# Optimization experiments

Measured on AMD Instinct MI355X. Metric: run time of the kernel, lower is better.

## Reference

```python
import jax, jax.numpy as jnp
import numpy as np

B, S, H, D = 2, 2048, 16, 128
HID = H * D
THETA = 10000.0
SCALE = 1.0 / np.sqrt(D)


def setup_inputs() -> dict:
    key = jax.random.key(0)
    k1, k2, k3 = jax.random.split(key, 3)
    x = jax.random.normal(k1, (B, S, HID), dtype=jnp.float32)
    w_qkv = jax.random.normal(k2, (3 * HID, HID), dtype=jnp.float32) * 0.02
    w_o = jax.random.normal(k3, (HID, HID), dtype=jnp.float32) * 0.02
    return {"x": x, "w_qkv": w_qkv, "w_o": w_o}


def _rope_cos_sin(seq_len, dim, dtype):
    inv_freq = 1.0 / (THETA ** (jnp.arange(0, dim, 2, dtype=jnp.float32) / dim))
    pos = jnp.arange(seq_len, dtype=jnp.float32)
    freqs = pos[:, None] * inv_freq[None, :]          # (S, D/2)
    emb = jnp.concatenate([freqs, freqs], axis=-1)    # (S, D)
    return jnp.cos(emb).astype(dtype), jnp.sin(emb).astype(dtype)


def _rotate_half(t):
    t1, t2 = jnp.split(t, 2, axis=-1)
    return jnp.concatenate([-t2, t1], axis=-1)


def reference(x, w_qkv, w_o):
    b, s, _ = x.shape
    qkv = jnp.einsum('bsh,oh->bso', x, w_qkv)                 # (B,S,3*HID)
    qkv = qkv.reshape(b, s, 3, H, D).transpose(2, 0, 3, 1, 4)  # (3,B,H,S,D)
    q, k, v = qkv[0], qkv[1], qkv[2]
    cos, sin = _rope_cos_sin(s, D, x.dtype)                    # (S,D)
    q = q * cos + _rotate_half(q) * sin
    k = k * cos + _rotate_half(k) * sin
    scores = jnp.einsum('bhqd,bhkd->bhqk', q, k) * SCALE       # (B,H,S,S)
    causal = jnp.triu(jnp.ones((s, s), dtype=bool), k=1)
    scores = jnp.where(causal[None, None], -jnp.inf, scores)
    attn = jax.nn.softmax(scores.astype(jnp.float32), axis=-1).astype(q.dtype)
    out = jnp.einsum('bhqk,bhkd->bhqd', attn, v)               # (B,H,S,D)
    out = out.transpose(0, 2, 1, 3).reshape(b, s, HID)
    return jnp.einsum('bsh,oh->bso', out, w_o)
```

## Files before the change

kernel.cpp:

```cpp
#include <hip/hip_runtime.h>
#include <hip/hip_bf16.h>

typedef unsigned short u16;
typedef unsigned long long u64;
typedef u16 us8 __attribute__((ext_vector_type(8)));
typedef __bf16 bf8_t __attribute__((ext_vector_type(8)));
typedef float f32x4 __attribute__((ext_vector_type(4)));

__device__ __forceinline__ float b2f(u16 u) {
    return __uint_as_float(((unsigned int)u) << 16);
}
__device__ __forceinline__ u16 f2b(float f) {
    union { __hip_bfloat16 h; u16 u; } v;
    v.h = __float2bfloat16(f);
    return v.u;
}
__device__ __forceinline__ f32x4 mfma16(bf8_t a, bf8_t b, f32x4 c) {
    return __builtin_amdgcn_mfma_f32_16x16x32_bf16(a, b, c, 0, 0, 0);
}
__device__ __forceinline__ void gload_lds16(const u16* g, u16* lds_base) {
    __builtin_amdgcn_global_load_lds((const __attribute__((address_space(1))) unsigned int*)g,
                                     (__attribute__((address_space(3))) unsigned int*)lds_base,
                                     16, 0, 0);
}

__global__ __launch_bounds__(256) void f32_to_bf16(const float* __restrict__ src,
                                                   u16* __restrict__ dst, int n8) {
    int idx = blockIdx.x * 256 + threadIdx.x;
    if (idx >= n8) return;
    float4 f0 = ((const float4*)src)[idx * 2];
    float4 f1 = ((const float4*)src)[idx * 2 + 1];
    us8 o;
    o[0] = f2b(f0.x); o[1] = f2b(f0.y); o[2] = f2b(f0.z); o[3] = f2b(f0.w);
    o[4] = f2b(f1.x); o[5] = f2b(f1.y); o[6] = f2b(f1.z); o[7] = f2b(f1.w);
    ((us8*)dst)[idx] = o;
}

template<int STORE_F32>
__global__ __launch_bounds__(256) void gemm_mfma_bt(const u16* __restrict__ A, const u16* __restrict__ B,
                                                    void* __restrict__ Cout, int M, int N, int K, int ldc) {
    __shared__ u16 Alds[128 * 32];
    __shared__ u16 Blds[128 * 32];
    const int tid = threadIdx.x;
    const int lane = tid & 63, wave = tid >> 6;
    const int lm = lane & 15, lq = lane >> 4;
    const int wm = wave >> 1, wn = wave & 1;
    const int m0 = blockIdx.y * 128, n0 = blockIdx.x * 128;
    const int srow = lane >> 2;
    const int scol = (lane & 3) * 8;

    f32x4 acc[4][4] = {};

    for (int k0 = 0; k0 < K; k0 += 32) {
#pragma unroll
        for (int p = 0; p < 2; p++) {
            int rbase = wave * 16 + p * 64;
            gload_lds16(A + (size_t)(m0 + rbase + srow) * K + k0 + scol, &Alds[rbase * 32]);
            gload_lds16(B + (size_t)(n0 + rbase + srow) * K + k0 + scol, &Blds[rbase * 32]);
        }
        __syncthreads();
        bf8_t af[4], bf[4];
#pragma unroll
        for (int mb = 0; mb < 4; mb++)
            af[mb] = *(const bf8_t*)&Alds[(wm * 64 + mb * 16 + lm) * 32 + lq * 8];
#pragma unroll
        for (int nb = 0; nb < 4; nb++)
            bf[nb] = *(const bf8_t*)&Blds[(wn * 64 + nb * 16 + lm) * 32 + lq * 8];
#pragma unroll
        for (int mb = 0; mb < 4; mb++)
#pragma unroll
            for (int nb = 0; nb < 4; nb++)
                acc[mb][nb] = mfma16(af[mb], bf[nb], acc[mb][nb]);
        __syncthreads();
    }
#pragma unroll
    for (int mb = 0; mb < 4; mb++)
#pragma unroll
        for (int nb = 0; nb < 4; nb++)
#pragma unroll
            for (int r = 0; r < 4; r++) {
                int row = m0 + wm * 64 + mb * 16 + lq * 4 + r;
                int col = n0 + wn * 64 + nb * 16 + lm;
                if (STORE_F32)
                    ((float*)Cout)[(size_t)row * ldc + col] = acc[mb][nb][r];
                else
                    ((u16*)Cout)[(size_t)row * ldc + col] = f2b(acc[mb][nb][r]);
            }
}

__global__ __launch_bounds__(256) void rope_bf16(u16* __restrict__ qkv) {
    int idx = blockIdx.x * 256 + threadIdx.x;
    int j = idx & 63;
    int h = (idx >> 6) & 15;
    int s = (idx >> 10) & 2047;
    int b = idx >> 21;
    size_t base = ((size_t)(b * 2048 + s)) * 6144 + h * 128;
    float inv = __expf((float)j * (-9.210340371976184f / 64.f));
    float ang = (float)s * inv;
    float sn, c;
    sincosf(ang, &sn, &c);
    float q1 = b2f(qkv[base + j]), q2 = b2f(qkv[base + j + 64]);
    qkv[base + j]      = f2b(q1 * c - q2 * sn);
    qkv[base + j + 64] = f2b(q2 * c + q1 * sn);
    float k1 = b2f(qkv[base + 2048 + j]), k2 = b2f(qkv[base + 2048 + j + 64]);
    qkv[base + 2048 + j]      = f2b(k1 * c - k2 * sn);
    qkv[base + 2048 + j + 64] = f2b(k2 * c + k1 * sn);
}

__global__ __launch_bounds__(256) void transpose_v(const u16* __restrict__ qkv, u16* __restrict__ VT) {
    __shared__ u16 T[64 * 136];
    const int tid = threadIdx.x;
    const int s0 = blockIdx.x * 64;
    const int bh = blockIdx.y;
    const int b = bh >> 4, h = bh & 15;
#pragma unroll
    for (int p = 0; p < 4; p++) {
        int sl = p * 16 + (tid >> 4);
        int d0 = (tid & 15) * 8;
        *(us8*)&T[sl * 136 + d0] =
            *(const us8*)(qkv + ((size_t)(b * 2048 + s0 + sl)) * 6144 + 4096 + h * 128 + d0);
    }
    __syncthreads();
#pragma unroll
    for (int p = 0; p < 4; p++) {
        int idx = p * 256 + tid;
        int d = idx & 127;
        int sg = idx >> 7;
        us8 v;
#pragma unroll
        for (int i = 0; i < 8; i++) v[i] = T[(sg * 8 + i) * 136 + d];
        *(us8*)&VT[((size_t)bh * 128 + d) * 2048 + s0 + sg * 8] = v;
    }
}

#define ATT_SCALE 0.08838834764831845f

__global__ __launch_bounds__(256) void attn_flash(const u16* __restrict__ qkv, const u16* __restrict__ VT,
                                                  u16* __restrict__ AO) {
    const int bh = blockIdx.x;
    const int qt = 31 - blockIdx.y;
    const int b = bh >> 4, h = bh & 15;
    const int tid = threadIdx.x, lane = tid & 63, wave = tid >> 6;
    const int lm = lane & 15, lq = lane >> 4;
    const int q0 = qt * 64;

    __shared__ u16 Kt[64 * 136];
    __shared__ u16 Vt[128 * 72];

    bf8_t qf[4];
    {
        const u16* Qrow = qkv + ((size_t)(b * 2048 + q0 + wave * 16 + lm)) * 6144 + h * 128;
#pragma unroll
        for (int ks = 0; ks < 4; ks++)
            qf[ks] = *(const bf8_t*)(Qrow + ks * 32 + lq * 8);
    }

    f32x4 Of[8] = {};
    float mrun = -3.0e38f, lrun = 0.f;

    const u16* Kbase = qkv + (size_t)b * 2048 * 6144 + 2048 + h * 128;
    const u16* VTbase = VT + (size_t)bh * 128 * 2048;

    const int krow = tid >> 4;
    const int kcol = (tid & 15) * 8;
    const int vrow = tid >> 3;
    const int vcol = (tid & 7) * 8;

    us8 kreg[4], vreg[4];
#pragma unroll
    for (int p = 0; p < 4; p++) {
        kreg[p] = *(const us8*)(Kbase + (size_t)(p * 16 + krow) * 6144 + kcol);
        vreg[p] = *(const us8*)(VTbase + (size_t)(p * 32 + vrow) * 2048 + vcol);
    }

    for (int kt = 0; kt <= qt; kt++) {
        __syncthreads();
#pragma unroll
        for (int p = 0; p < 4; p++) {
            *(us8*)&Kt[(p * 16 + krow) * 136 + kcol] = kreg[p];
            *(us8*)&Vt[(p * 32 + vrow) * 72 + vcol] = vreg[p];
        }
        __syncthreads();
        {
            int kn = (kt + 1 <= qt ? kt + 1 : qt) * 64;
#pragma unroll
            for (int p = 0; p < 4; p++) {
                kreg[p] = *(const us8*)(Kbase + (size_t)(kn + p * 16 + krow) * 6144 + kcol);
                vreg[p] = *(const us8*)(VTbase + (size_t)(p * 32 + vrow) * 2048 + kn + vcol);
            }
        }

        float sv[4][4];
#pragma unroll
        for (int nb = 0; nb < 4; nb++) {
            f32x4 a = {};
#pragma unroll
            for (int ks = 0; ks < 4; ks++) {
                bf8_t kf = *(const bf8_t*)&Kt[(nb * 16 + lm) * 136 + ks * 32 + lq * 8];
                a = mfma16(kf, qf[ks], a);
            }
#pragma unroll
            for (int r = 0; r < 4; r++) sv[nb][r] = a[r] * ATT_SCALE;
        }
        if (kt == qt) {
            int qloc = wave * 16 + lm;
#pragma unroll
            for (int nb = 0; nb < 4; nb++)
#pragma unroll
                for (int r = 0; r < 4; r++)
                    if (nb * 16 + lq * 4 + r > qloc) sv[nb][r] = -3.0e38f;
        }
        float mx = -3.0e38f;
#pragma unroll
        for (int nb = 0; nb < 4; nb++)
#pragma unroll
            for (int r = 0; r < 4; r++) mx = fmaxf(mx, sv[nb][r]);
        mx = fmaxf(mx, __shfl_xor(mx, 16, 64));
        mx = fmaxf(mx, __shfl_xor(mx, 32, 64));
        float mnew = fmaxf(mrun, mx);
        float alpha = __expf(mrun - mnew);
        float rs = 0.f;
        u64 pk[4];
#pragma unroll
        for (int nb = 0; nb < 4; nb++) {
            float e0 = __expf(sv[nb][0] - mnew), e1 = __expf(sv[nb][1] - mnew);
            float e2 = __expf(sv[nb][2] - mnew), e3 = __expf(sv[nb][3] - mnew);
            rs += (e0 + e1) + (e2 + e3);
            unsigned int lo = (unsigned int)f2b(e0) | ((unsigned int)f2b(e1) << 16);
            unsigned int hi = (unsigned int)f2b(e2) | ((unsigned int)f2b(e3) << 16);
            pk[nb] = (u64)lo | ((u64)hi << 32);
        }
        rs += __shfl_xor(rs, 16, 64);
        rs += __shfl_xor(rs, 32, 64);
        lrun = lrun * alpha + rs;
        mrun = mnew;
#pragma unroll
        for (int db = 0; db < 8; db++)
#pragma unroll
            for (int r = 0; r < 4; r++) Of[db][r] *= alpha;

        const int slo = ((lq & 1) * 2) * 16 + lm;
        const int shi = slo + 16;
        const bool sel = (lq >> 1) != 0;
#pragma unroll
        for (int kk = 0; kk < 2; kk++) {
            u64 lo0 = __shfl(pk[2 * kk + 0], slo, 64);
            u64 lo1 = __shfl(pk[2 * kk + 1], slo, 64);
            u64 hi0 = __shfl(pk[2 * kk + 0], shi, 64);
            u64 hi1 = __shfl(pk[2 * kk + 1], shi, 64);
            union { u64 v[2]; bf8_t f; } pf;
            pf.v[0] = sel ? lo1 : lo0;
            pf.v[1] = sel ? hi1 : hi0;
#pragma unroll
            for (int db = 0; db < 8; db++) {
                bf8_t vf = *(const bf8_t*)&Vt[(db * 16 + lm) * 72 + kk * 32 + lq * 8];
                Of[db] = mfma16(vf, pf.f, Of[db]);
            }
        }
    }
    float invl = 1.f / lrun;
    size_t rowbase = (size_t)(b * 2048 + q0 + wave * 16 + lm) * 2048 + h * 128;
#pragma unroll
    for (int db = 0; db < 8; db++) {
        ushort4 o;
        o.x = f2b(Of[db][0] * invl);
        o.y = f2b(Of[db][1] * invl);
        o.z = f2b(Of[db][2] * invl);
        o.w = f2b(Of[db][3] * invl);
        *(ushort4*)(AO + rowbase + db * 16 + lq * 4) = o;
    }
}

extern "C" void kernel_launch(void* const* d_in, const int* in_sizes, int n_in,
                              void* d_out, int out_size, void* d_ws, size_t ws_size,
                              hipStream_t stream) {
    const float* x     = (const float*)d_in[0];
    const float* w_qkv = (const float*)d_in[1];
    const float* w_o   = (const float*)d_in[2];
    float* out = (float*)d_out;
    u16* ws = (u16*)d_ws;

    u16* qkvb  = ws;
    u16* VT    = ws + 25165824;
    u16* AO    = ws + 33554432;
    u16* xb    = ws + 41943040;
    u16* wqkvb = ws + 50331648;
    u16* wob   = ws + 62914560;

    f32_to_bf16<<<4096, 256, 0, stream>>>(x, xb, 1048576);
    f32_to_bf16<<<6144, 256, 0, stream>>>(w_qkv, wqkvb, 1572864);
    f32_to_bf16<<<2048, 256, 0, stream>>>(w_o, wob, 524288);
    gemm_mfma_bt<0><<<dim3(48, 32), 256, 0, stream>>>(xb, wqkvb, qkvb, 4096, 6144, 2048, 6144);
    rope_bf16<<<16384, 256, 0, stream>>>(qkvb);
    transpose_v<<<dim3(32, 32), 256, 0, stream>>>(qkvb, VT);
    attn_flash<<<dim3(32, 32), 256, 0, stream>>>(qkvb, VT, AO);
    gemm_mfma_bt<1><<<dim3(16, 32), 256, 0, stream>>>(AO, wob, out, 4096, 2048, 2048, 2048);
}
```

Before: 423.2 us.

## Fuse RoPE into V transpose and read K/V directly from global in attention

Merges the RoPE pass into the V-transpose kernel, using vectorized 8-element loads/stores and fast sincos, which removes one launch and a strided scalar pass. The attention kernel drops LDS staging, barriers and register prefetch of K and V tiles, and loads MFMA operands straight from global memory. This removes the synchronization and LDS traffic, but each wave now fetches the same K/V data redundantly with strided access and no prefetch.

New measurement: 585.9 us. 1.38x slower.

```diff
diff --git a/kernel.cpp b/kernel.cpp
--- a/kernel.cpp
+++ b/kernel.cpp
@@ -88,26 +88,7 @@
             }
 }
 
-__global__ __launch_bounds__(256) void rope_bf16(u16* __restrict__ qkv) {
-    int idx = blockIdx.x * 256 + threadIdx.x;
-    int j = idx & 63;
-    int h = (idx >> 6) & 15;
-    int s = (idx >> 10) & 2047;
-    int b = idx >> 21;
-    size_t base = ((size_t)(b * 2048 + s)) * 6144 + h * 128;
-    float inv = __expf((float)j * (-9.210340371976184f / 64.f));
-    float ang = (float)s * inv;
-    float sn, c;
-    sincosf(ang, &sn, &c);
-    float q1 = b2f(qkv[base + j]), q2 = b2f(qkv[base + j + 64]);
-    qkv[base + j]      = f2b(q1 * c - q2 * sn);
-    qkv[base + j + 64] = f2b(q2 * c + q1 * sn);
-    float k1 = b2f(qkv[base + 2048 + j]), k2 = b2f(qkv[base + 2048 + j + 64]);
-    qkv[base + 2048 + j]      = f2b(k1 * c - k2 * sn);
-    qkv[base + 2048 + j + 64] = f2b(k2 * c + k1 * sn);
-}
-
-__global__ __launch_bounds__(256) void transpose_v(const u16* __restrict__ qkv, u16* __restrict__ VT) {
+__global__ __launch_bounds__(256) void rope_vt(u16* __restrict__ qkv, u16* __restrict__ VT) {
     __shared__ u16 T[64 * 136];
     const int tid = threadIdx.x;
     const int s0 = blockIdx.x * 64;
@@ -119,6 +100,37 @@
         int d0 = (tid & 15) * 8;
         *(us8*)&T[sl * 136 + d0] =
             *(const us8*)(qkv + ((size_t)(b * 2048 + s0 + sl)) * 6144 + 4096 + h * 128 + d0);
+    }
+#pragma unroll
+    for (int p = 0; p < 2; p++) {
+        int task = p * 256 + tid;
+        int sl = task >> 3;
+        int jg = task & 7;
+        size_t base = ((size_t)(b * 2048 + s0 + sl)) * 6144 + h * 128 + jg * 8;
+        us8 qlo = *(const us8*)(qkv + base);
+        us8 qhi = *(const us8*)(qkv + base + 64);
+        us8 klo = *(const us8*)(qkv + base + 2048);
+        us8 khi = *(const us8*)(qkv + base + 2048 + 64);
+        us8 oql, oqh, okl, okh;
+        float s = (float)(s0 + sl);
+#pragma unroll
+        for (int e = 0; e < 8; e++) {
+            int j = jg * 8 + e;
+            float inv = __expf((float)j * (-9.210340371976184f / 64.f));
+            float ang = s * inv;
+            float sn, c;
+            __sincosf(ang, &sn, &c);
+            float q1 = b2f(qlo[e]), q2 = b2f(qhi[e]);
+            oql[e] = f2b(q1 * c - q2 * sn);
+            oqh[e] = f2b(q2 * c + q1 * sn);
+            float k1 = b2f(klo[e]), k2 = b2f(khi[e]);
+            okl[e] = f2b(k1 * c - k2 * sn);
+            okh[e] = f2b(k2 * c + k1 * sn);
+        }
+        *(us8*)(qkv + base) = oql;
+        *(us8*)(qkv + base + 64) = oqh;
+        *(us8*)(qkv + base + 2048) = okl;
+        *(us8*)(qkv + base + 2048 + 64) = okh;
     }
     __syncthreads();
 #pragma unroll
@@ -144,9 +156,6 @@
     const int lm = lane & 15, lq = lane >> 4;
     const int q0 = qt * 64;
 
-    __shared__ u16 Kt[64 * 136];
-    __shared__ u16 Vt[128 * 72];
-
     bf8_t qf[4];
     {
         const u16* Qrow = qkv + ((size_t)(b * 2048 + q0 + wave * 16 + lm)) * 6144 + h * 128;
@@ -158,45 +167,19 @@
     f32x4 Of[8] = {};
     float mrun = -3.0e38f, lrun = 0.f;
 
-    const u16* Kbase = qkv + (size_t)b * 2048 * 6144 + 2048 + h * 128;
-    const u16* VTbase = VT + (size_t)bh * 128 * 2048;
-
-    const int krow = tid >> 4;
-    const int kcol = (tid & 15) * 8;
-    const int vrow = tid >> 3;
-    const int vcol = (tid & 7) * 8;
-
-    us8 kreg[4], vreg[4];
-#pragma unroll
-    for (int p = 0; p < 4; p++) {
-        kreg[p] = *(const us8*)(Kbase + (size_t)(p * 16 + krow) * 6144 + kcol);
-        vreg[p] = *(const us8*)(VTbase + (size_t)(p * 32 + vrow) * 2048 + vcol);
-    }
+    const u16* Kbase = qkv + (size_t)b * 2048 * 6144 + 2048 + h * 128 + lq * 8;
+    const u16* VTb = VT + (size_t)bh * 128 * 2048 + lq * 8;
 
     for (int kt = 0; kt <= qt; kt++) {
-        __syncthreads();
-#pragma unroll
-        for (int p = 0; p < 4; p++) {
-            *(us8*)&Kt[(p * 16 + krow) * 136 + kcol] = kreg[p];
-            *(us8*)&Vt[(p * 32 + vrow) * 72 + vcol] = vreg[p];
-        }
-        __syncthreads();
-        {
-            int kn = (kt + 1 <= qt ? kt + 1 : qt) * 64;
-#pragma unroll
-            for (int p = 0; p < 4; p++) {
-                kreg[p] = *(const us8*)(Kbase + (size_t)(kn + p * 16 + krow) * 6144 + kcol);
-                vreg[p] = *(const us8*)(VTbase + (size_t)(p * 32 + vrow) * 2048 + kn + vcol);
-            }
-        }
-
+        const int k0 = kt * 64;
         float sv[4][4];
 #pragma unroll
         for (int nb = 0; nb < 4; nb++) {
+            const u16* Krow = Kbase + (size_t)(k0 + nb * 16 + lm) * 6144;
             f32x4 a = {};
 #pragma unroll
             for (int ks = 0; ks < 4; ks++) {
-                bf8_t kf = *(const bf8_t*)&Kt[(nb * 16 + lm) * 136 + ks * 32 + lq * 8];
+                bf8_t kf = *(const bf8_t*)(Krow + ks * 32);
                 a = mfma16(kf, qf[ks], a);
             }
 #pragma unroll
@@ -251,9 +234,10 @@
             union { u64 v[2]; bf8_t f; } pf;
             pf.v[0] = sel ? lo1 : lo0;
             pf.v[1] = sel ? hi1 : hi0;
+            const u16* Vcol = VTb + k0 + kk * 32;
 #pragma unroll
             for (int db = 0; db < 8; db++) {
-                bf8_t vf = *(const bf8_t*)&Vt[(db * 16 + lm) * 72 + kk * 32 + lq * 8];
+                bf8_t vf = *(const bf8_t*)(Vcol + (size_t)(db * 16 + lm) * 2048);
                 Of[db] = mfma16(vf, pf.f, Of[db]);
             }
         }
@@ -291,8 +275,7 @@
     f32_to_bf16<<<6144, 256, 0, stream>>>(w_qkv, wqkvb, 1572864);
     f32_to_bf16<<<2048, 256, 0, stream>>>(w_o, wob, 524288);
     gemm_mfma_bt<0><<<dim3(48, 32), 256, 0, stream>>>(xb, wqkvb, qkvb, 4096, 6144, 2048, 6144);
-    rope_bf16<<<16384, 256, 0, stream>>>(qkvb);
-    transpose_v<<<dim3(32, 32), 256, 0, stream>>>(qkvb, VT);
+    rope_vt<<<dim3(32, 32), 256, 0, stream>>>(qkvb, VT);
     attn_flash<<<dim3(32, 32), 256, 0, stream>>>(qkvb, VT, AO);
     gemm_mfma_bt<1><<<dim3(16, 32), 256, 0, stream>>>(AO, wob, out, 4096, 2048, 2048, 2048);
 }
```
